# Kernel optimization log

Measured on AMD Instinct MI355X. Metric: run time of the kernel, lower is better.

Reference implementation:

```python
import jax, jax.numpy as jnp
import numpy as np

DIM = 256
HEADS = 8
HEAD_DIM = DIM // HEADS
SCALE = HEAD_DIM ** -0.5
WD, WH, WW = 2, 7, 7
N = WD * WH * WW            # 98 tokens per window
NW = 256                    # windows per sample
B = 2048                    # batch * num_windows
PBT_LEN = (2 * WD - 1) * (2 * WH - 1) * (2 * WW - 1)  # 507


def _relative_position_index():
    # Deterministic buffer from __init__: [N, N] int indices into pbt rows.
    coords = np.stack(np.meshgrid(np.arange(WD), np.arange(WH), np.arange(WW), indexing='ij'))
    coords = coords.reshape(3, -1)                      # [3, N]
    rel = coords[:, :, None] - coords[:, None, :]       # [3, N, N]
    rel = rel.transpose(1, 2, 0).copy()                 # [N, N, 3]
    rel[..., 0] += WD - 1
    rel[..., 1] += WH - 1
    rel[..., 2] += WW - 1
    rel[..., 0] *= (2 * WH - 1) * (2 * WW - 1)
    rel[..., 1] *= 2 * WW - 1
    return rel.sum(-1)                                  # [N, N]


def setup_inputs() -> dict:
    key = jax.random.key(0)
    ks = jax.random.split(key, 6)
    x = jax.random.normal(ks[0], (B, N, DIM), dtype=jnp.float32)
    mask = jax.random.normal(ks[1], (NW, N, N), dtype=jnp.float32)
    pbt = jax.random.normal(ks[2], (PBT_LEN, HEADS), dtype=jnp.float32) * 0.02
    qkv_w = jax.random.normal(ks[3], (3 * DIM, DIM), dtype=jnp.float32) * 0.02
    proj_w = jax.random.normal(ks[4], (DIM, DIM), dtype=jnp.float32) * 0.02
    proj_b = jax.random.normal(ks[5], (DIM,), dtype=jnp.float32) * 0.02
    rpi = jnp.asarray(_relative_position_index(), dtype=jnp.int32)
    return {"x": x, "mask": mask, "pbt": pbt, "qkv_w": qkv_w,
            "proj_w": proj_w, "proj_b": proj_b, "rpi": rpi}


def reference(x, mask, pbt, qkv_w, proj_w, proj_b, rpi):
    b, n, c = x.shape
    qkv = x @ qkv_w.T                                   # [b, n, 3c] (qkv_bias=False)
    q, k, v = jnp.split(qkv, 3, axis=-1)
    to_heads = lambda t: t.reshape(b, n, HEADS, HEAD_DIM).transpose(0, 2, 1, 3)
    q, k, v = to_heads(q), to_heads(k), to_heads(v)     # [b, h, n, d]

    attn = SCALE * jnp.einsum('bhnd,bhmd->bhnm', q, k)  # [b, h, n, n]
    # gathered relative-position bias: pbt[rpi] -> [n, n, h] -> [h, n, n]
    bias = pbt[rpi.reshape(-1)].reshape(n, n, HEADS).transpose(2, 0, 1)
    attn = attn + bias[None]

    n_w = mask.shape[0]
    attn = attn.reshape(b // n_w, n_w, HEADS, n, n) + mask[None, :, None]
    attn = attn.reshape(b, HEADS, n, n)

    attn = jax.nn.softmax(attn, axis=-1)
    out = jnp.einsum('bhnm,bhmd->bhnd', attn, v)        # [b, h, n, d]
    out = out.transpose(0, 2, 1, 3).reshape(b, n, c)
    return out @ proj_w.T + proj_b
```

## Files before the change

### kernel.cpp

```cpp
#include <hip/hip_runtime.h>
#include <hip/hip_bf16.h>
#include <math.h>

typedef float f32x4 __attribute__((ext_vector_type(4)));
typedef __bf16 bf16x8 __attribute__((ext_vector_type(8)));

#define NTOK 98
#define NWIN 2048
#define NN (NTOK * NTOK)
#define SCALE 0.17677669529663689f
#define MROWS (NWIN * NTOK)
#define PSTRIDE 9408

__device__ __forceinline__ void g2l16(const void* g, void* l) {
  typedef __attribute__((address_space(1))) const unsigned int GU;
  typedef __attribute__((address_space(3))) unsigned int LU;
  __builtin_amdgcn_global_load_lds((GU*)g, (LU*)l, 16, 0, 0);
}

__global__ void prep_kernel(const float* __restrict__ qkv_w, const float* __restrict__ proj_w,
                            const float* __restrict__ pbt, const int* __restrict__ rpi,
                            const float* __restrict__ mask,
                            __bf16* __restrict__ qkvw_b, __bf16* __restrict__ projw_b,
                            float* __restrict__ cmb) {
  int i = blockIdx.x * 256 + threadIdx.x;
  if (i < 768 * 256) qkvw_b[i] = (__bf16)qkv_w[i];
  if (i < 256 * 256) projw_b[i] = (__bf16)proj_w[i];
  if (i < 256 * 8 * NTOK * 128) {
    int mh = i / (NTOK * 128);
    int rem = i - mh * (NTOK * 128);
    int row = rem >> 7, j = rem & 127;
    if (j < NTOK) {
      int m = mh >> 3, h = mh & 7;
      cmb[i] = pbt[rpi[row * NTOK + j] * 8 + h] + mask[m * NN + row * NTOK + j];
    } else {
      cmb[i] = 0.f;
    }
  }
}

__launch_bounds__(256)
__global__ void gemm_qkv(const float* __restrict__ A, const __bf16* __restrict__ W,
                         __bf16* __restrict__ C) {
  __shared__ __align__(16) char As[65536];
  __shared__ __align__(16) char Bs[2][8192];
  const int m0 = blockIdx.x * 128;
  const int tid = threadIdx.x;
  const int lane = tid & 63;
  const int wid = tid >> 6;
  const int wm = wid & 1, wn = wid >> 1;
  const int lr = lane & 15;
  const int lg = lane >> 4;

  for (int c = tid; c < 128 * 32; c += 256) {
    int row = c >> 5, slot = c & 31;
    const float* ap = A + (size_t)(m0 + row) * 256 + slot * 8;
    float4 f0 = *(const float4*)ap;
    float4 f1 = *(const float4*)(ap + 4);
    bf16x8 hv;
    hv[0] = (__bf16)f0.x; hv[1] = (__bf16)f0.y; hv[2] = (__bf16)f0.z; hv[3] = (__bf16)f0.w;
    hv[4] = (__bf16)f1.x; hv[5] = (__bf16)f1.y; hv[6] = (__bf16)f1.z; hv[7] = (__bf16)f1.w;
    *(bf16x8*)(As + row * 512 + ((slot * 16) ^ ((row & 7) << 4))) = hv;
  }
  __syncthreads();

  for (int nt = 0; nt < 6; ++nt) {
    const int n0 = nt * 128;
    f32x4 acc[4][4] = {};

#pragma unroll
    for (int it2 = 0; it2 < 2; ++it2) {
      int wc = wid * 2 + it2;
      int cc = wc * 64 + lane;
      int row = cc >> 2, slot = cc & 3;
      int sw = (row & 3) ^ ((row >> 3) & 3);
      g2l16(W + (size_t)(n0 + row) * 256 + ((slot ^ sw) * 8), (void*)(Bs[0] + wc * 1024));
    }
    __syncthreads();

    for (int ks = 0; ks < 8; ++ks) {
      const int cur = ks & 1;
      if (ks < 7) {
#pragma unroll
        for (int it2 = 0; it2 < 2; ++it2) {
          int wc = wid * 2 + it2;
          int cc = wc * 64 + lane;
          int row = cc >> 2, slot = cc & 3;
          int sw = (row & 3) ^ ((row >> 3) & 3);
          g2l16(W + (size_t)(n0 + row) * 256 + (ks + 1) * 32 + ((slot ^ sw) * 8),
                (void*)(Bs[cur ^ 1] + wc * 1024));
        }
      }
      bf16x8 a[4], b[4];
#pragma unroll
      for (int m = 0; m < 4; ++m) {
        int row = wm * 64 + m * 16 + lr;
        a[m] = *(const bf16x8*)(As + row * 512 + ((ks * 64 + lg * 16) ^ ((row & 7) << 4)));
      }
#pragma unroll
      for (int n = 0; n < 4; ++n) {
        int row = wn * 64 + n * 16 + lr;
        int sw = (row & 3) ^ ((row >> 3) & 3);
        b[n] = *(const bf16x8*)(Bs[cur] + row * 64 + ((lg * 16) ^ (sw << 4)));
      }
#pragma unroll
      for (int m = 0; m < 4; ++m)
#pragma unroll
        for (int n = 0; n < 4; ++n)
          acc[m][n] = __builtin_amdgcn_mfma_f32_16x16x32_bf16(a[m], b[n], acc[m][n], 0, 0, 0);
      __syncthreads();
    }

#pragma unroll
    for (int m = 0; m < 4; ++m)
#pragma unroll
      for (int r = 0; r < 4; ++r) {
        unsigned row = m0 + wm * 64 + m * 16 + lg * 4 + r;
        unsigned win = row / NTOK;
        unsigned tok = row - win * NTOK;
#pragma unroll
        for (int n = 0; n < 4; ++n) {
          int col = n0 + wn * 64 + n * 16 + lr;
          int sec = col >> 8, dd = col & 255;
          int h = dd >> 5, d = dd & 31;
          C[(size_t)(win * 8 + h) * PSTRIDE + (size_t)sec * 3136 + tok * 32 + d] =
              (__bf16)acc[m][n][r];
        }
      }
  }
}

__launch_bounds__(128)
__global__ void attn_kernel(const __bf16* __restrict__ qkv, const float* __restrict__ cmb,
                            __bf16* __restrict__ y) {
  __shared__ __align__(16) char VTB[8192];
  int bx = blockIdx.x;
  int lb = (bx & 7) * 2048 + (bx >> 3);
  const int win = lb >> 3, h = lb & 7;
  const int tid = threadIdx.x;
  const int lane = tid & 63, wv = tid >> 6;
  const int lr = lane & 15, lg = lane >> 4;
  const f32x4 fz = {0.f, 0.f, 0.f, 0.f};

  const __bf16* qw = qkv + (size_t)(win * 8 + h) * PSTRIDE;
  const __bf16* kw = qw + 3136;
  const __bf16* vw = qw + 6272;
  const float* cw = cmb + (size_t)((win & 255) * 8 + h) * (NTOK * 128);

  for (int c = tid; c < 512; c += 128) {
    int j = c & 127; int jc = j < NTOK ? j : NTOK - 1;
    int d8 = (c >> 7) << 3;
    bf16x8 vv = *(const bf16x8*)(vw + jc * 32 + d8);
#pragma unroll
    for (int e = 0; e < 8; ++e) {
      int d = d8 + e;
      *(__bf16*)(VTB + d * 256 + ((2 * j) ^ ((d & 7) << 4))) = vv[e];
    }
  }

  bf16x8 bk[7];
#pragma unroll
  for (int jt = 0; jt < 7; ++jt) {
    int brow = ((jt >> 1) << 5) + ((lr >> 2) << 3) + ((jt & 1) << 2) + (lr & 3);
    int browc = brow < NTOK ? brow : NTOK - 1;
    bk[jt] = *(const bf16x8*)(kw + browc * 32 + lg * 8);
  }
  __syncthreads();

  for (int it = wv; it < 7; it += 2) {
    const int i0 = it * 16;
    const int qrow = i0 + lr;
    const int qrowc = qrow < NTOK ? qrow : NTOK - 1;
    bf16x8 aq = *(const bf16x8*)(qw + qrowc * 32 + lg * 8);

    const float* cr = cw + qrowc * 128;
    float4 cv[7];
#pragma unroll
    for (int jt = 0; jt < 7; ++jt) {
      int kb = ((jt >> 1) << 5) + lg * 8 + ((jt & 1) << 2);
      cv[jt] = *(const float4*)(cr + kb);
    }

    f32x4 s[7];
#pragma unroll
    for (int jt = 0; jt < 7; ++jt)
      s[jt] = __builtin_amdgcn_mfma_f32_16x16x32_bf16(bk[jt], aq, fz, 0, 0, 0);

    float sv[7][4];
    float mx = -INFINITY;
#pragma unroll
    for (int jt = 0; jt < 7; ++jt) {
      int kb = ((jt >> 1) << 5) + lg * 8 + ((jt & 1) << 2);
#pragma unroll
      for (int r = 0; r < 4; ++r) {
        float xv = (kb + r < NTOK) ? fmaf(SCALE, s[jt][r], (&cv[jt].x)[r]) : -INFINITY;
        sv[jt][r] = xv;
        mx = fmaxf(mx, xv);
      }
    }
    mx = fmaxf(mx, __shfl_xor(mx, 16));
    mx = fmaxf(mx, __shfl_xor(mx, 32));
    float sum = 0.f;
#pragma unroll
    for (int jt = 0; jt < 7; ++jt)
#pragma unroll
      for (int r = 0; r < 4; ++r) {
        float p = __expf(sv[jt][r] - mx);
        sv[jt][r] = p;
        sum += p;
      }
    sum += __shfl_xor(sum, 16);
    sum += __shfl_xor(sum, 32);
    const float rinv = 1.f / sum;

    bf16x8 pa[4];
#pragma unroll
    for (int ks = 0; ks < 4; ++ks)
#pragma unroll
      for (int e = 0; e < 8; ++e) {
        int jt = 2 * ks + (e >> 2);
        pa[ks][e] = (jt < 7) ? (__bf16)sv[jt][e & 3] : (__bf16)0.f;
      }

    float rv[4];
#pragma unroll
    for (int r = 0; r < 4; ++r) rv[r] = __shfl(rinv, lg * 4 + r);

#pragma unroll
    for (int dt = 0; dt < 2; ++dt) {
      f32x4 o = fz;
#pragma unroll
      for (int ks = 0; ks < 4; ++ks) {
        int vrow = dt * 16 + lr;
        bf16x8 vb = *(const bf16x8*)(VTB + vrow * 256 + ((ks * 64 + lg * 16) ^ ((vrow & 7) << 4)));
        o = __builtin_amdgcn_mfma_f32_16x16x32_bf16(pa[ks], vb, o, 0, 0, 0);
      }
#pragma unroll
      for (int r = 0; r < 4; ++r) {
        int row = i0 + lg * 4 + r;
        if (row < NTOK)
          y[((size_t)win * NTOK + row) * 256 + h * 32 + dt * 16 + lr] = (__bf16)(o[r] * rv[r]);
      }
    }
  }
}

__launch_bounds__(256)
__global__ void gemm_proj(const __bf16* __restrict__ A, const __bf16* __restrict__ W,
                          const float* __restrict__ pb, float* __restrict__ C) {
  __shared__ __align__(16) char As[128 * 128];
  __shared__ __align__(16) char Bs[128 * 128];
  const int bid = blockIdx.x;
  const int m0 = (bid / 2) * 128;
  const int n0 = (bid % 2) * 128;
  const int tid = threadIdx.x;
  const int lane = tid & 63;
  const int wid = tid >> 6;
  const int wm = wid & 1, wn = wid >> 1;
  const int lr = lane & 15;
  const int lg = lane >> 4;
  f32x4 acc[4][4] = {};

  for (int k0 = 0; k0 < 256; k0 += 64) {
#pragma unroll
    for (int it = 0; it < 4; ++it) {
      int c = wid * 4 + it;
      int row = c * 8 + (lane >> 3);
      int src_chunk = (lane & 7) ^ (row & 7);
      g2l16(A + (size_t)(m0 + row) * 256 + k0 + src_chunk * 8, (void*)(As + c * 1024));
      g2l16(W + (size_t)(n0 + row) * 256 + k0 + src_chunk * 8, (void*)(Bs + c * 1024));
    }
    __syncthreads();
#pragma unroll
    for (int kk = 0; kk < 2; ++kk) {
      bf16x8 a[4], b[4];
#pragma unroll
      for (int m = 0; m < 4; ++m) {
        int row = wm * 64 + m * 16 + lr;
        a[m] = *(const bf16x8*)(As + row * 128 + ((kk * 64 + lg * 16) ^ ((row & 7) << 4)));
      }
#pragma unroll
      for (int n = 0; n < 4; ++n) {
        int row = wn * 64 + n * 16 + lr;
        b[n] = *(const bf16x8*)(Bs + row * 128 + ((kk * 64 + lg * 16) ^ ((row & 7) << 4)));
      }
#pragma unroll
      for (int m = 0; m < 4; ++m)
#pragma unroll
        for (int n = 0; n < 4; ++n)
          acc[m][n] = __builtin_amdgcn_mfma_f32_16x16x32_bf16(a[m], b[n], acc[m][n], 0, 0, 0);
    }
    __syncthreads();
  }
#pragma unroll
  for (int m = 0; m < 4; ++m) {
    int row = m0 + wm * 64 + m * 16 + lg * 4;
#pragma unroll
    for (int n = 0; n < 4; ++n) {
      int col = n0 + wn * 64 + n * 16 + lr;
      float bv = pb[col];
#pragma unroll
      for (int r = 0; r < 4; ++r)
        C[(size_t)(row + r) * 256 + col] = acc[m][n][r] + bv;
    }
  }
}

extern "C" void kernel_launch(void* const* d_in, const int* in_sizes, int n_in,
                              void* d_out, int out_size, void* d_ws, size_t ws_size,
                              hipStream_t stream) {
  const float* x      = (const float*)d_in[0];
  const float* mask   = (const float*)d_in[1];
  const float* pbt    = (const float*)d_in[2];
  const float* qkv_w  = (const float*)d_in[3];
  const float* proj_w = (const float*)d_in[4];
  const float* proj_b = (const float*)d_in[5];
  const int*   rpi    = (const int*)d_in[6];
  float* out = (float*)d_out;

  char* ws = (char*)d_ws;
  __bf16* qkv      = (__bf16*)(ws);
  __bf16* y        = (__bf16*)(ws + 308281344);
  __bf16* qkvw_b   = (__bf16*)(ws + 411041792);
  __bf16* projw_b  = (__bf16*)(ws + 411435008);
  float*  cmb      = (float*) (ws + 411566080);

  int prep_n = 256 * 8 * NTOK * 128;
  prep_kernel<<<(prep_n + 255) / 256, 256, 0, stream>>>(qkv_w, proj_w, pbt, rpi, mask,
                                                        qkvw_b, projw_b, cmb);
  gemm_qkv<<<MROWS / 128, 256, 0, stream>>>(x, qkvw_b, qkv);
  attn_kernel<<<NWIN * 8, 128, 0, stream>>>(qkv, cmb, y);
  gemm_proj<<<(MROWS / 128) * 2, 256, 0, stream>>>(y, projw_b, proj_b, out);
}
```

Measured before the change: 509.5 us.

## Overlap bias/mask table build with QKV GEMM and restructure projection GEMM

The combined bias+mask table construction moves out of the prep kernel into odd-numbered blocks of the QKV GEMM launch, where it runs concurrently with the GEMM blocks and writes float4 stores. The prep kernel now only converts weights to bf16. The projection GEMM now keeps a full 128x256 A tile resident in LDS, loops over both N halves, and double-buffers weight K-slices. This halves A re-reads across blocks, at the cost of larger LDS use per block and lower occupancy.

```diff
diff --git a/kernel.cpp b/kernel.cpp
--- a/kernel.cpp
+++ b/kernel.cpp
@@ -18,34 +18,44 @@
   __builtin_amdgcn_global_load_lds((GU*)g, (LU*)l, 16, 0, 0);
 }
 
-__global__ void prep_kernel(const float* __restrict__ qkv_w, const float* __restrict__ proj_w,
-                            const float* __restrict__ pbt, const int* __restrict__ rpi,
-                            const float* __restrict__ mask,
-                            __bf16* __restrict__ qkvw_b, __bf16* __restrict__ projw_b,
-                            float* __restrict__ cmb) {
+__global__ void prep_w_kernel(const float* __restrict__ qkv_w, const float* __restrict__ proj_w,
+                              __bf16* __restrict__ qkvw_b, __bf16* __restrict__ projw_b) {
   int i = blockIdx.x * 256 + threadIdx.x;
   if (i < 768 * 256) qkvw_b[i] = (__bf16)qkv_w[i];
   if (i < 256 * 256) projw_b[i] = (__bf16)proj_w[i];
-  if (i < 256 * 8 * NTOK * 128) {
-    int mh = i / (NTOK * 128);
-    int rem = i - mh * (NTOK * 128);
-    int row = rem >> 7, j = rem & 127;
-    if (j < NTOK) {
-      int m = mh >> 3, h = mh & 7;
-      cmb[i] = pbt[rpi[row * NTOK + j] * 8 + h] + mask[m * NN + row * NTOK + j];
-    } else {
-      cmb[i] = 0.f;
-    }
-  }
 }
 
 __launch_bounds__(256)
-__global__ void gemm_qkv(const float* __restrict__ A, const __bf16* __restrict__ W,
-                         __bf16* __restrict__ C) {
+__global__ void gemm_cmb_kernel(const float* __restrict__ A, const __bf16* __restrict__ W,
+                                __bf16* __restrict__ C,
+                                const float* __restrict__ pbt, const int* __restrict__ rpi,
+                                const float* __restrict__ mask, float* __restrict__ cmb) {
   __shared__ __align__(16) char As[65536];
   __shared__ __align__(16) char Bs[2][8192];
-  const int m0 = blockIdx.x * 128;
   const int tid = threadIdx.x;
+
+  if (blockIdx.x & 1) {
+    const int cb = blockIdx.x >> 1;
+#pragma unroll 4
+    for (int s = 0; s < 16; ++s) {
+      int fidx = cb * 4096 + s * 256 + tid;
+      int e = fidx * 4;
+      int mh = e / 12544;
+      int rem = e - mh * 12544;
+      int row = rem >> 7, j = rem & 127;
+      int m = mh >> 3, h = mh & 7;
+      const float* mrow = mask + (size_t)m * NN + row * NTOK;
+      const int* rrow = rpi + row * NTOK;
+      float4 v;
+#pragma unroll
+      for (int c = 0; c < 4; ++c)
+        (&v.x)[c] = (j + c < NTOK) ? pbt[rrow[j + c] * 8 + h] + mrow[j + c] : 0.f;
+      *(float4*)(cmb + e) = v;
+    }
+    return;
+  }
+
+  const int m0 = (blockIdx.x >> 1) * 128;
   const int lane = tid & 63;
   const int wid = tid >> 6;
   const int wm = wid & 1, wn = wid >> 1;
@@ -248,60 +258,84 @@
 __launch_bounds__(256)
 __global__ void gemm_proj(const __bf16* __restrict__ A, const __bf16* __restrict__ W,
                           const float* __restrict__ pb, float* __restrict__ C) {
-  __shared__ __align__(16) char As[128 * 128];
-  __shared__ __align__(16) char Bs[128 * 128];
-  const int bid = blockIdx.x;
-  const int m0 = (bid / 2) * 128;
-  const int n0 = (bid % 2) * 128;
+  __shared__ __align__(16) char As[65536];
+  __shared__ __align__(16) char Bs[2][8192];
+  const int m0 = blockIdx.x * 128;
   const int tid = threadIdx.x;
   const int lane = tid & 63;
   const int wid = tid >> 6;
   const int wm = wid & 1, wn = wid >> 1;
   const int lr = lane & 15;
   const int lg = lane >> 4;
-  f32x4 acc[4][4] = {};
-
-  for (int k0 = 0; k0 < 256; k0 += 64) {
-#pragma unroll
-    for (int it = 0; it < 4; ++it) {
-      int c = wid * 4 + it;
-      int row = c * 8 + (lane >> 3);
-      int src_chunk = (lane & 7) ^ (row & 7);
-      g2l16(A + (size_t)(m0 + row) * 256 + k0 + src_chunk * 8, (void*)(As + c * 1024));
-      g2l16(W + (size_t)(n0 + row) * 256 + k0 + src_chunk * 8, (void*)(Bs + c * 1024));
+
+#pragma unroll
+  for (int it = 0; it < 16; ++it) {
+    int c = wid * 16 + it;
+    int cc = c * 64 + lane;
+    int row = cc >> 5, slot = cc & 31;
+    int src = slot ^ (row & 7);
+    g2l16(A + (size_t)(m0 + row) * 256 + src * 8, (void*)(As + c * 1024));
+  }
+  __syncthreads();
+
+  for (int nt = 0; nt < 2; ++nt) {
+    const int n0 = nt * 128;
+    f32x4 acc[4][4] = {};
+
+#pragma unroll
+    for (int it2 = 0; it2 < 2; ++it2) {
+      int wc = wid * 2 + it2;
+      int cc = wc * 64 + lane;
+      int row = cc >> 2, slot = cc & 3;
+      int sw = (row & 3) ^ ((row >> 3) & 3);
+      g2l16(W + (size_t)(n0 + row) * 256 + ((slot ^ sw) * 8), (void*)(Bs[0] + wc * 1024));
     }
     __syncthreads();
-#pragma unroll
-    for (int kk = 0; kk < 2; ++kk) {
+
+    for (int ks = 0; ks < 8; ++ks) {
+      const int cur = ks & 1;
+      if (ks < 7) {
+#pragma unroll
+        for (int it2 = 0; it2 < 2; ++it2) {
+          int wc = wid * 2 + it2;
+          int cc = wc * 64 + lane;
+          int row = cc >> 2, slot = cc & 3;
+          int sw = (row & 3) ^ ((row >> 3) & 3);
+          g2l16(W + (size_t)(n0 + row) * 256 + (ks + 1) * 32 + ((slot ^ sw) * 8),
+                (void*)(Bs[cur ^ 1] + wc * 1024));
+        }
+      }
       bf16x8 a[4], b[4];
 #pragma unroll
       for (int m = 0; m < 4; ++m) {
         int row = wm * 64 + m * 16 + lr;
-        a[m] = *(const bf16x8*)(As + row * 128 + ((kk * 64 + lg * 16) ^ ((row & 7) << 4)));
+        a[m] = *(const bf16x8*)(As + row * 512 + ((ks * 64 + lg * 16) ^ ((row & 7) << 4)));
       }
 #pragma unroll
       for (int n = 0; n < 4; ++n) {
         int row = wn * 64 + n * 16 + lr;
-        b[n] = *(const bf16x8*)(Bs + row * 128 + ((kk * 64 + lg * 16) ^ ((row & 7) << 4)));
+        int sw = (row & 3) ^ ((row >> 3) & 3);
+        b[n] = *(const bf16x8*)(Bs[cur] + row * 64 + ((lg * 16) ^ (sw << 4)));
       }
 #pragma unroll
       for (int m = 0; m < 4; ++m)
 #pragma unroll
         for (int n = 0; n < 4; ++n)
           acc[m][n] = __builtin_amdgcn_mfma_f32_16x16x32_bf16(a[m], b[n], acc[m][n], 0, 0, 0);
-    }
-    __syncthreads();
-  }
-#pragma unroll
-  for (int m = 0; m < 4; ++m) {
-    int row = m0 + wm * 64 + m * 16 + lg * 4;
-#pragma unroll
-    for (int n = 0; n < 4; ++n) {
-      int col = n0 + wn * 64 + n * 16 + lr;
-      float bv = pb[col];
-#pragma unroll
-      for (int r = 0; r < 4; ++r)
-        C[(size_t)(row + r) * 256 + col] = acc[m][n][r] + bv;
+      __syncthreads();
+    }
+
+#pragma unroll
+    for (int m = 0; m < 4; ++m) {
+      int row = m0 + wm * 64 + m * 16 + lg * 4;
+#pragma unroll
+      for (int n = 0; n < 4; ++n) {
+        int col = n0 + wn * 64 + n * 16 + lr;
+        float bv = pb[col];
+#pragma unroll
+        for (int r = 0; r < 4; ++r)
+          C[(size_t)(row + r) * 256 + col] = acc[m][n][r] + bv;
+      }
     }
   }
 }
@@ -325,10 +359,8 @@
   __bf16* projw_b  = (__bf16*)(ws + 411435008);
   float*  cmb      = (float*) (ws + 411566080);
 
-  int prep_n = 256 * 8 * NTOK * 128;
-  prep_kernel<<<(prep_n + 255) / 256, 256, 0, stream>>>(qkv_w, proj_w, pbt, rpi, mask,
-                                                        qkvw_b, projw_b, cmb);
-  gemm_qkv<<<MROWS / 128, 256, 0, stream>>>(x, qkvw_b, qkv);
+  prep_w_kernel<<<768, 256, 0, stream>>>(qkv_w, proj_w, qkvw_b, projw_b);
+  gemm_cmb_kernel<<<(MROWS / 128) * 2, 256, 0, stream>>>(x, qkvw_b, qkv, pbt, rpi, mask, cmb);
   attn_kernel<<<NWIN * 8, 128, 0, stream>>>(qkv, cmb, y);
-  gemm_proj<<<(MROWS / 128) * 2, 256, 0, stream>>>(y, projw_b, proj_b, out);
-}
+  gemm_proj<<<MROWS / 128, 256, 0, stream>>>(y, projw_b, proj_b, out);
+}
```

Measured after the change: 537.0 us. +5.4%, slower.
